# Kernel tuning notes

Hardware: AMD Instinct MI355X
Metric: run time of the kernel (lower is better)

The kernel has to match this reference:

```python
import jax, jax.numpy as jnp
import numpy as np

B, T0, H0, W0 = 16, 8, 14, 14
DIM = 768
HEADS = 8
HD = DIM // HEADS  # 96
N = T0 * H0 * W0 + 1  # 1569 (cls token)
STRIDE_Q = (1, 1, 1)
STRIDE_KV = (1, 2, 2)
REL_SP_DIM = 2 * max(H0, H0 // 2) - 1  # 27
REL_T_DIM = 2 * T0 - 1  # 15
LN_EPS = 1e-5


def _rel_idx(q, k):
    # decomposed relative-position index table (static, numpy)
    q_ratio = max(k / q, 1.0)
    k_ratio = max(q / k, 1.0)
    d = np.arange(q)[:, None] * q_ratio - np.arange(k)[None, :] * k_ratio
    d += (k - 1) * k_ratio
    return d.astype(np.int64)


def _layernorm(x, g, b):
    m = jnp.mean(x, axis=-1, keepdims=True)
    v = jnp.mean((x - m) ** 2, axis=-1, keepdims=True)
    return (x - m) * jax.lax.rsqrt(v + LN_EPS) * g + b


def _attention_pool(t, w, thw, stride, g, b):
    # t: [B, heads, 1+L, C]; depthwise 3x3x3 conv over THW, cls token bypasses pool
    cls_tok, body = t[:, :, :1], t[:, :, 1:]
    Bb, NH, L, C = body.shape
    T, H, W = thw
    x = body.reshape(Bb * NH, T, H, W, C).transpose(0, 4, 1, 2, 3)  # NCDHW
    y = jax.lax.conv_general_dilated(
        x, w, window_strides=stride, padding=[(1, 1), (1, 1), (1, 1)],
        feature_group_count=C, dimension_numbers=('NCDHW', 'OIDHW', 'NCDHW'))
    nT, nH, nW = y.shape[2], y.shape[3], y.shape[4]
    y = y.reshape(Bb, NH, C, nT * nH * nW).transpose(0, 1, 3, 2)
    y = jnp.concatenate([cls_tok, y], axis=2)
    return _layernorm(y, g, b), (nT, nH, nW)


def setup_inputs() -> dict:
    key = jax.random.key(0)
    ks = jax.random.split(key, 12)
    s = 0.02
    inp = {
        'x': jax.random.normal(ks[0], (B, N, DIM), jnp.float32),
        'qkv_w': jax.random.normal(ks[1], (DIM, 3 * DIM), jnp.float32) * s,
        'qkv_b': jax.random.normal(ks[2], (3 * DIM,), jnp.float32) * s,
        'pool_q_w': jax.random.normal(ks[3], (HD, 1, 3, 3, 3), jnp.float32) * s,
        'pool_k_w': jax.random.normal(ks[4], (HD, 1, 3, 3, 3), jnp.float32) * s,
        'pool_v_w': jax.random.normal(ks[5], (HD, 1, 3, 3, 3), jnp.float32) * s,
        'ln_q_g': jnp.ones((HD,), jnp.float32), 'ln_q_b': jnp.zeros((HD,), jnp.float32),
        'ln_k_g': jnp.ones((HD,), jnp.float32), 'ln_k_b': jnp.zeros((HD,), jnp.float32),
        'ln_v_g': jnp.ones((HD,), jnp.float32), 'ln_v_b': jnp.zeros((HD,), jnp.float32),
        'rel_pos_h': jax.random.normal(ks[6], (REL_SP_DIM, HD), jnp.float32) * s,
        'rel_pos_w': jax.random.normal(ks[7], (REL_SP_DIM, HD), jnp.float32) * s,
        'rel_pos_t': jax.random.normal(ks[8], (REL_T_DIM, HD), jnp.float32) * s,
        'proj_w': jax.random.normal(ks[9], (DIM, DIM), jnp.float32) * s,
        'proj_b': jax.random.normal(ks[10], (DIM,), jnp.float32) * s,
        'thw_t': T0, 'thw_h': H0, 'thw_w': W0,
    }
    return inp


def reference(x, qkv_w, qkv_b, pool_q_w, pool_k_w, pool_v_w,
              ln_q_g, ln_q_b, ln_k_g, ln_k_b, ln_v_g, ln_v_b,
              rel_pos_h, rel_pos_w, rel_pos_t, proj_w, proj_b,
              thw_t, thw_h, thw_w):
    thw = (int(thw_t), int(thw_h), int(thw_w))
    Bb, Nn, _ = x.shape
    qkv = (x @ qkv_w + qkv_b).reshape(Bb, Nn, 3, HEADS, HD).transpose(2, 0, 3, 1, 4)
    q, k, v = qkv[0], qkv[1], qkv[2]  # [B, H, N, hd]
    q, q_shape = _attention_pool(q, pool_q_w, thw, STRIDE_Q, ln_q_g, ln_q_b)
    k, k_shape = _attention_pool(k, pool_k_w, thw, STRIDE_KV, ln_k_g, ln_k_b)
    v, _ = _attention_pool(v, pool_v_w, thw, STRIDE_KV, ln_v_g, ln_v_b)
    qt, qh, qw = q_shape
    kt, kh, kw = k_shape
    scale = HD ** -0.5
    attn = jnp.einsum('bhqc,bhkc->bhqk', q * scale, k)  # [B,H,1+Lq,1+Lk]
    # spatial + temporal decomposed relative position bias (cls row/col excluded)
    Rh = rel_pos_h[_rel_idx(qh, kh)]  # [qh,kh,hd]
    Rw = rel_pos_w[_rel_idx(qw, kw)]  # [qw,kw,hd]
    Rt = rel_pos_t[_rel_idx(qt, kt)]  # [qt,kt,hd]
    r_q = q[:, :, 1:].reshape(Bb, HEADS, qt, qh, qw, HD)
    rel_h = jnp.einsum('bythwc,hkc->bythwk', r_q, Rh)  # [B,H,qt,qh,qw,kh]
    rel_w = jnp.einsum('bythwc,wkc->bythwk', r_q, Rw)  # [B,H,qt,qh,qw,kw]
    rel_t = jnp.einsum('bnthwc,tkc->bnthwk', r_q, Rt)  # [B,H,qt,qh,qw,kt]
    bias = (rel_h[:, :, :, :, :, None, :, None]
            + rel_w[:, :, :, :, :, None, None, :]
            + rel_t[:, :, :, :, :, :, None, None])  # [B,H,qt,qh,qw,kt,kh,kw]
    attn = attn.at[:, :, 1:, 1:].add(bias.reshape(Bb, HEADS, qt * qh * qw, kt * kh * kw))
    attn = jax.nn.softmax(attn, axis=-1)
    out = jnp.einsum('bhqk,bhkc->bhqc', attn, v)
    out = out.at[:, :, 1:].add(q[:, :, 1:])  # residual pooling (skip cls)
    out = out.transpose(0, 2, 1, 3).reshape(Bb, -1, DIM)
    out = out @ proj_w + proj_b
    return out
```

## Files before the change

### kernel.cpp

```cpp
#include <hip/hip_runtime.h>
#include <hip/hip_bf16.h>

typedef __hip_bfloat16 bf16;
typedef __attribute__((ext_vector_type(8))) short bf16x8;
typedef __attribute__((ext_vector_type(4))) float f32x4;

#define B_     16
#define N_     1569
#define DIM_   768
#define NHEADS 8
#define HD_    96
#define LK_    393
#define T0_    8
#define H0_    14
#define W0_    14

struct __align__(8) bf16x4s { bf16 a, b, c, d; };

__device__ __forceinline__ float b2f(unsigned short u) {
  union { unsigned int i; float f; } x;
  x.i = ((unsigned int)u) << 16;
  return x.f;
}

__global__ __launch_bounds__(256) void cvt_f32_bf16(
    const float* __restrict__ in, bf16* __restrict__ out, int n4) {
  int i = blockIdx.x * 256 + threadIdx.x;
  if (i < n4) {
    float4 v = ((const float4*)in)[i];
    bf16x4s o{__float2bfloat16(v.x), __float2bfloat16(v.y),
              __float2bfloat16(v.z), __float2bfloat16(v.w)};
    ((bf16x4s*)out)[i] = o;
  }
}

__global__ __launch_bounds__(256) void transpose_f32_bf16(
    const float* __restrict__ in, bf16* __restrict__ out, int R, int C) {
  __shared__ float tile[32][33];
  int c0 = blockIdx.x * 32, r0 = blockIdx.y * 32;
  int tx = threadIdx.x, ty = threadIdx.y;
  for (int i = 0; i < 32; i += 8) {
    int r = r0 + ty + i, c = c0 + tx;
    if (r < R && c < C) tile[ty + i][tx] = in[(size_t)r * C + c];
  }
  __syncthreads();
  for (int i = 0; i < 32; i += 8) {
    int c = c0 + ty + i, r = r0 + tx;
    if (c < C && r < R) out[(size_t)c * R + r] = __float2bfloat16(tile[tx][ty + i]);
  }
}

__global__ __launch_bounds__(256) void prep_pw(
    const float* __restrict__ wq, const float* __restrict__ wk,
    const float* __restrict__ wv, float* __restrict__ outp) {
  int i = blockIdx.x * 256 + threadIdx.x;
  if (i < 2592) {
    int widx = i / 96, x = i % 96;
    outp[i]        = wq[x * 27 + widx];
    outp[2592 + i] = wk[x * 27 + widx];
    outp[5184 + i] = wv[x * 27 + widx];
  }
}

__device__ __forceinline__ void gl_lds16(const bf16* g, bf16* l) {
  __builtin_amdgcn_global_load_lds(
      (const __attribute__((address_space(1))) void*)g,
      (__attribute__((address_space(3))) void*)l, 16, 0, 0);
}

template <typename OutT>
__global__ __launch_bounds__(256) void gemm_bt(
    const bf16* __restrict__ A, const bf16* __restrict__ BT,
    const float* __restrict__ bias, OutT* __restrict__ C,
    int M, int Nn, int K) {
  constexpr int BM = 128, BN = 128, BK = 64;
  __shared__ __align__(16) bf16 As[BM][BK];
  __shared__ __align__(16) bf16 Bs[BN][BK];
  const int tid = threadIdx.x;
  const int lane = tid & 63, wave = tid >> 6;

  const int nNp = Nn >> 7;
  const int nwg = gridDim.x;
  const int q8 = nwg >> 3, r8 = nwg & 7;
  const int xcd = blockIdx.x & 7, idx = blockIdx.x >> 3;
  const int w = (xcd < r8 ? xcd * (q8 + 1) : r8 * (q8 + 1) + (xcd - r8) * q8) + idx;
  const int bm = (w / nNp) * BM, bn = (w % nNp) * BN;

  const int wm = (wave >> 1) * 64, wn = (wave & 1) * 64;
  const int sl = lane >> 3;
  const int sc = ((lane & 7) ^ sl) * 8;

  f32x4 acc[4][4];
#pragma unroll
  for (int i = 0; i < 4; ++i)
#pragma unroll
    for (int j = 0; j < 4; ++j) acc[i][j] = (f32x4){0.f, 0.f, 0.f, 0.f};

  for (int k0 = 0; k0 < K; k0 += BK) {
#pragma unroll
    for (int c = 0; c < 4; ++c) {
      int r0 = wave * 32 + c * 8;
      int arow = bm + r0 + sl;
      if (arow >= M) arow = M - 1;
      gl_lds16(A + (size_t)arow * K + k0 + sc, &As[r0][0]);
      int brow = bn + r0 + sl;
      gl_lds16(BT + (size_t)brow * K + k0 + sc, &Bs[r0][0]);
    }
    __syncthreads();
    const int fr = lane & 15, q = lane >> 4;
#pragma unroll
    for (int ks = 0; ks < 2; ++ks) {
      const int ph = (((ks << 2) + q) ^ (fr & 7)) << 3;
      bf16x8 af[4], bfr[4];
#pragma unroll
      for (int i = 0; i < 4; ++i) {
        af[i] = *(const bf16x8*)&As[wm + i * 16 + fr][ph];
        bfr[i] = *(const bf16x8*)&Bs[wn + i * 16 + fr][ph];
      }
#pragma unroll
      for (int i = 0; i < 4; ++i)
#pragma unroll
        for (int j = 0; j < 4; ++j)
          acc[i][j] = __builtin_amdgcn_mfma_f32_16x16x32_bf16(af[i], bfr[j],
                                                              acc[i][j], 0, 0, 0);
    }
    __syncthreads();
  }

  const int fr = lane & 15, rg = (lane >> 4) * 4;
#pragma unroll
  for (int j = 0; j < 4; ++j) {
    int col = bn + wn + j * 16 + fr;
    float bv = bias[col];
#pragma unroll
    for (int i = 0; i < 4; ++i) {
#pragma unroll
      for (int r = 0; r < 4; ++r) {
        int row = bm + wm + i * 16 + rg + r;
        if (row < M)
          C[(size_t)row * Nn + col] = (OutT)(acc[i][j][r] + bv);
      }
    }
  }
}

__global__ __launch_bounds__(256) void pool_ln(
    const bf16* __restrict__ qkv, const float* __restrict__ pwT,
    const float* __restrict__ g, const float* __restrict__ bt,
    bf16* __restrict__ outp, int which, int sHW, int oH, int oW, int Lout) {
  __shared__ float pwl[27 * 104];
  const int tid = threadIdx.x;
  for (int i = tid; i < 2592; i += 256) {
    int widx = i / 96, c = i % 96;
    int cgi = c >> 3, j = c & 7;
    pwl[widx * 104 + cgi * 8 + (cgi >> 2) * 4 + j] = pwT[i];
  }
  __syncthreads();

  const int rloc = tid >> 4;
  const int cg = tid & 15;
  const int orow = blockIdx.x * 16 + rloc;
  if (orow >= Lout) return;
  const int bh = blockIdx.y;
  const int b = bh >> 3, h = bh & 7;
  const bool act = (cg < 12);
  const bf16* base =
      qkv + (size_t)b * N_ * 2304 + which * 768 + h * 96 + cg * 8;

  float acc[8];
#pragma unroll
  for (int j = 0; j < 8; ++j) acc[j] = 0.f;

  if (act) {
    if (orow == 0) {
      union { uint4 u; bf16 e[8]; } tv;
      tv.u = *(const uint4*)base;
#pragma unroll
      for (int j = 0; j < 8; ++j) acc[j] = (float)tv.e[j];
    } else {
      int pos = orow - 1;
      int ot = pos / (oH * oW), r = pos % (oH * oW);
      int oh = r / oW, ow = r % oW;
      const float* wrow = pwl + cg * 8 + (cg >> 2) * 4;
#pragma unroll
      for (int kt = 0; kt < 3; ++kt) {
        int it = ot + kt - 1;
        if (it < 0 || it >= T0_) continue;
#pragma unroll
        for (int kh = 0; kh < 3; ++kh) {
          int ih = oh * sHW + kh - 1;
          if (ih < 0 || ih >= H0_) continue;
#pragma unroll
          for (int kw = 0; kw < 3; ++kw) {
            int iw = ow * sHW + kw - 1;
            if (iw < 0 || iw >= W0_) continue;
            int n = 1 + (it * H0_ + ih) * W0_ + iw;
            int widx = (kt * 3 + kh) * 3 + kw;
            union { uint4 u; bf16 e[8]; } tv;
            tv.u = *(const uint4*)(base + (size_t)n * 2304);
            const float* w = wrow + widx * 104;
            float wv_[8];
            *(float4*)&wv_[0] = *(const float4*)w;
            *(float4*)&wv_[4] = *(const float4*)(w + 4);
#pragma unroll
            for (int j = 0; j < 8; ++j) acc[j] += (float)tv.e[j] * wv_[j];
          }
        }
      }
    }
  }

  float s = 0.f, s2 = 0.f;
#pragma unroll
  for (int j = 0; j < 8; ++j) { s += acc[j]; s2 += acc[j] * acc[j]; }
#pragma unroll
  for (int mk = 1; mk < 16; mk <<= 1) {
    s += __shfl_xor(s, mk);
    s2 += __shfl_xor(s2, mk);
  }
  float mean = s * (1.f / 96.f);
  float var = s2 * (1.f / 96.f) - mean * mean;
  float rstd = rsqrtf(var + 1e-5f);

  if (act) {
    float gv[8], bv[8];
    *(float4*)&gv[0] = *(const float4*)(g + cg * 8);
    *(float4*)&gv[4] = *(const float4*)(g + cg * 8 + 4);
    *(float4*)&bv[0] = *(const float4*)(bt + cg * 8);
    *(float4*)&bv[4] = *(const float4*)(bt + cg * 8 + 4);
    union { uint4 u; bf16 e[8]; } ov;
#pragma unroll
    for (int j = 0; j < 8; ++j)
      ov.e[j] = __float2bfloat16((acc[j] - mean) * rstd * gv[j] + bv[j]);
    *(uint4*)(outp + ((size_t)bh * Lout + orow) * 96 + cg * 8) = ov.u;
  }
}

__global__ __launch_bounds__(256) void vtran(
    const bf16* __restrict__ vp, bf16* __restrict__ vt) {
  __shared__ __align__(16) bf16 tile[64][104];
  const int tid = threadIdx.x;
  const int bh = blockIdx.y, kt0 = blockIdx.x * 64;
  const bf16* src = vp + (size_t)bh * LK_ * HD_;
  for (int c = tid; c < 768; c += 256) {
    int row = c / 12, seg = c % 12;
    int key = kt0 + row;
    uint4 v = {0u, 0u, 0u, 0u};
    if (key < LK_) v = *(const uint4*)(src + (size_t)key * HD_ + seg * 8);
    *(uint4*)&tile[row][seg * 8] = v;
  }
  __syncthreads();
  bf16* dst = vt + (size_t)bh * 96 * 448 + kt0;
  for (int c = tid; c < 768; c += 256) {
    int d = c >> 3, ch = c & 7;
    union { uint4 u; bf16 e[8]; } o;
#pragma unroll
    for (int j = 0; j < 8; ++j) o.e[j] = tile[ch * 8 + j][d];
    *(uint4*)(dst + (size_t)d * 448 + ch * 8) = o.u;
  }
}

__global__ __launch_bounds__(256) void rel_dots(
    const bf16* __restrict__ qp, const float* __restrict__ rpt,
    const float* __restrict__ rph, const float* __restrict__ rpw,
    float* __restrict__ relq) {
  __shared__ float tab[69 * 100];
  __shared__ __align__(16) bf16 Qls[64][96];
  const int tid = threadIdx.x;
  const int bh = blockIdx.y;
  const int q0 = blockIdx.x * 64;
  const bf16* qb = qp + (size_t)bh * N_ * HD_;

  for (int i = tid; i < 69 * 24; i += 256) {
    int row = i / 24, c4 = (i % 24) * 4;
    const float* src = row < 15 ? rpt + row * 96
                      : row < 42 ? rph + (row - 15) * 96
                                 : rpw + (row - 42) * 96;
    *(float4*)&tab[row * 100 + c4] = *(const float4*)(src + c4);
  }
  for (int c = tid; c < 768; c += 256) {
    int row = c / 12, seg = c % 12;
    int p = q0 + row;
    if (p >= N_) p = N_ - 1;
    *(uint4*)&Qls[row][seg * 8] = *(const uint4*)(qb + (size_t)p * HD_ + seg * 8);
  }
  __syncthreads();

  const int r8 = tid >> 5, slot = tid & 31;
  if (slot == 15 || slot >= 23) return;
  for (int g = 0; g < 8; ++g) {
    int row = g * 8 + r8;
    int p = q0 + row;
    if (p < 1 || p >= N_) continue;
    int pos = p - 1;
    int qt = pos / 196, rr = pos % 196;
    int qh = rr / 14, qw = rr % 14;
    int ti = slot < 8 ? qt - slot + 7
            : slot < 15 ? 15 + (qh - 2 * (slot - 8) + 12)
                        : 42 + (qw - 2 * (slot - 16) + 12);
    const float* trow = &tab[ti * 100];
    float acc = 0.f;
#pragma unroll
    for (int d4 = 0; d4 < 24; ++d4) {
      float4 w = *(const float4*)(trow + d4 * 4);
      union { uint2 u; unsigned short s[4]; } qv;
      qv.u = *(const uint2*)&Qls[row][d4 * 4];
      acc += w.x * b2f(qv.s[0]) + w.y * b2f(qv.s[1]) +
             w.z * b2f(qv.s[2]) + w.w * b2f(qv.s[3]);
    }
    relq[((size_t)bh * N_ + p) * 24 + slot] = acc;
  }
}

__global__ __launch_bounds__(256) void attn_fused(
    const bf16* __restrict__ qp, const bf16* __restrict__ kp,
    const bf16* __restrict__ vtb, const float* __restrict__ relq,
    bf16* __restrict__ aout) {
  __shared__ __align__(16) char smem[31744];
  bf16 (*Ks)[104]    = (bf16(*)[104])smem;
  bf16* VtS          = (bf16*)(smem + 13312);
  float (*relb)[24]  = (float(*)[24])(smem + 25600);
  bf16 (*Ps)[16][72] = (bf16(*)[16][72])smem;

  const int tid = threadIdx.x;
  const int wv = tid >> 6, lane = tid & 63;
  const int col = lane & 15, quad = lane >> 4;
  const int bh = blockIdx.y;
  const int b = bh >> 3;
  const int h = bh & 7;
  const int q0 = blockIdx.x * 64;
  const bf16* qb = qp + (size_t)bh * N_ * HD_;
  const bf16* kb = kp + (size_t)bh * LK_ * HD_;
  const bf16* vt = vtb + (size_t)bh * 96 * 448;
  const float scale = 0.102062072615966f;

  {
    int nrow = N_ - q0;
    if (nrow > 64) nrow = 64;
    int n4 = nrow * 6;
    const uint4* src = (const uint4*)(relq + ((size_t)bh * N_ + q0) * 24);
    for (int i = tid; i < n4; i += 256) ((uint4*)relb)[i] = src[i];
  }

  int qrow = q0 + wv * 16 + col;
  if (qrow >= N_) qrow = N_ - 1;
  bf16x8 qa[3];
#pragma unroll
  for (int ks_ = 0; ks_ < 3; ++ks_)
    qa[ks_] = *(const bf16x8*)(qb + (size_t)qrow * HD_ + ks_ * 32 + quad * 8);

  float mrun[4] = {-1e30f, -1e30f, -1e30f, -1e30f};
  float lrun[4] = {0.f, 0.f, 0.f, 0.f};
  f32x4 oacc[6];
#pragma unroll
  for (int dt = 0; dt < 6; ++dt) oacc[dt] = (f32x4){0.f, 0.f, 0.f, 0.f};

  for (int kt_i = 0; kt_i < 7; ++kt_i) {
    const int kt0 = kt_i * 64;
    __syncthreads();
    for (int c = tid; c < 768; c += 256) {
      int row = c / 12, seg = c % 12;
      int key = kt0 + row;
      if (key >= LK_) key = LK_ - 1;
      *(uint4*)&Ks[row][seg * 8] =
          *(const uint4*)(kb + (size_t)key * HD_ + seg * 8);
    }
    for (int c = tid; c < 768; c += 256) {
      int d = c >> 3, ch = c & 7;
      int c_ = (d ^ (d >> 3)) & 7;
      *(uint4*)&VtS[d * 64 + ch * 8] =
          *(const uint4*)(vt + (size_t)d * 448 + kt0 + ((ch ^ c_) * 8));
    }
    __syncthreads();

    f32x4 sacc[4];
#pragma unroll
    for (int jt = 0; jt < 4; ++jt) sacc[jt] = (f32x4){0.f, 0.f, 0.f, 0.f};
#pragma unroll
    for (int ks_ = 0; ks_ < 3; ++ks_) {
#pragma unroll
      for (int jt = 0; jt < 4; ++jt) {
        bf16x8 bk = *(const bf16x8*)&Ks[jt * 16 + col][ks_ * 32 + quad * 8];
        sacc[jt] = __builtin_amdgcn_mfma_f32_16x16x32_bf16(qa[ks_], bk, sacc[jt], 0, 0, 0);
      }
    }

    float sv[4][4];
#pragma unroll
    for (int jt = 0; jt < 4; ++jt) {
      int kglob = kt0 + jt * 16 + col;
      bool kvalid = (kglob < LK_);
      int kbod = (kglob >= 1) ? kglob - 1 : 0;
      int kt_ = kbod / 49, krem = kbod % 49;
      int kh_ = krem / 7, kw_ = krem % 7;
#pragma unroll
      for (int r = 0; r < 4; ++r) {
        int qr = wv * 16 + quad * 4 + r;
        int p = q0 + qr;
        float s = sacc[jt][r] * scale;
        if (kvalid && kglob >= 1 && p >= 1 && p < N_)
          s += relb[qr][kt_] + relb[qr][8 + kh_] + relb[qr][16 + kw_];
        if (!kvalid) s = -1e30f;
        sv[jt][r] = s;
      }
    }

    float pexp[4][4];
#pragma unroll
    for (int r = 0; r < 4; ++r) {
      float pm = fmaxf(fmaxf(sv[0][r], sv[1][r]), fmaxf(sv[2][r], sv[3][r]));
#pragma unroll
      for (int mk = 1; mk < 16; mk <<= 1) pm = fmaxf(pm, __shfl_xor(pm, mk));
      float mn = fmaxf(mrun[r], pm);
      float alpha = __expf(mrun[r] - mn);
      mrun[r] = mn;
      float rs = 0.f;
#pragma unroll
      for (int jt = 0; jt < 4; ++jt) {
        float e = __expf(sv[jt][r] - mn);
        pexp[jt][r] = e;
        rs += e;
      }
#pragma unroll
      for (int mk = 1; mk < 16; mk <<= 1) rs += __shfl_xor(rs, mk);
      lrun[r] = lrun[r] * alpha + rs;
#pragma unroll
      for (int dt = 0; dt < 6; ++dt) {
        oacc[dt][r] *= alpha;
      }
    }

    __syncthreads();

#pragma unroll
    for (int jt = 0; jt < 4; ++jt)
#pragma unroll
      for (int r = 0; r < 4; ++r)
        Ps[wv][quad * 4 + r][jt * 16 + col] = __float2bfloat16(pexp[jt][r]);

#pragma unroll
    for (int ks_ = 0; ks_ < 2; ++ks_) {
      bf16x8 ap = *(const bf16x8*)&Ps[wv][col][ks_ * 32 + quad * 8];
#pragma unroll
      for (int dt = 0; dt < 6; ++dt) {
        int d = dt * 16 + col;
        int c_ = (d ^ (d >> 3)) & 7;
        bf16x8 bv =
            *(const bf16x8*)&VtS[d * 64 + ((ks_ * 32 + quad * 8) ^ (c_ << 3))];
        oacc[dt] = __builtin_amdgcn_mfma_f32_16x16x32_bf16(ap, bv, oacc[dt], 0, 0, 0);
      }
    }
  }

#pragma unroll
  for (int r = 0; r < 4; ++r) {
    int qr = wv * 16 + quad * 4 + r;
    int p = q0 + qr;
    if (p >= N_) continue;
    float inv = 1.f / lrun[r];
#pragma unroll
    for (int dt = 0; dt < 6; ++dt) {
      int d = dt * 16 + col;
      float val = oacc[dt][r] * inv;
      if (p >= 1) val += (float)qb[(size_t)p * HD_ + d];
      aout[((size_t)b * N_ + p) * DIM_ + h * HD_ + d] = __float2bfloat16(val);
    }
  }
}

extern "C" void kernel_launch(void* const* d_in, const int* in_sizes, int n_in,
                              void* d_out, int out_size, void* d_ws,
                              size_t ws_size, hipStream_t stream) {
  (void)in_sizes; (void)n_in; (void)out_size; (void)ws_size;
  const float* x      = (const float*)d_in[0];
  const float* qkv_w  = (const float*)d_in[1];
  const float* qkv_b  = (const float*)d_in[2];
  const float* pool_q = (const float*)d_in[3];
  const float* pool_k = (const float*)d_in[4];
  const float* pool_v = (const float*)d_in[5];
  const float* ln_q_g = (const float*)d_in[6];
  const float* ln_q_b = (const float*)d_in[7];
  const float* ln_k_g = (const float*)d_in[8];
  const float* ln_k_b = (const float*)d_in[9];
  const float* ln_v_g = (const float*)d_in[10];
  const float* ln_v_b = (const float*)d_in[11];
  const float* rph    = (const float*)d_in[12];
  const float* rpw    = (const float*)d_in[13];
  const float* rpt    = (const float*)d_in[14];
  const float* proj_w = (const float*)d_in[15];
  const float* proj_b = (const float*)d_in[16];

  char* ws = (char*)d_ws;
  bf16* wt_qkv  = (bf16*)(ws);
  bf16* wt_proj = (bf16*)(ws + 3538944);
  bf16* xb      = (bf16*)(ws + 4718592);
  bf16* aout    = xb;
  bf16* qkv     = (bf16*)(ws + 43278336);
  float* relq   = (float*)(ws + 43278336);
  bf16* vtb     = (bf16*)(ws + 63278336);
  bf16* qpoolb  = (bf16*)(ws + 158957568);
  bf16* kpoolb  = (bf16*)(ws + 197517312);
  bf16* vpoolb  = (bf16*)(ws + 207175680);
  float* pwT    = (float*)(ws + 216834048);
  float* outp   = (float*)d_out;

  int n4 = (B_ * N_ * DIM_) / 4;
  cvt_f32_bf16<<<(n4 + 255) / 256, 256, 0, stream>>>(x, xb, n4);
  transpose_f32_bf16<<<dim3(72, 24), dim3(32, 8), 0, stream>>>(qkv_w, wt_qkv, 768, 2304);
  transpose_f32_bf16<<<dim3(24, 24), dim3(32, 8), 0, stream>>>(proj_w, wt_proj, 768, 768);
  prep_pw<<<11, 256, 0, stream>>>(pool_q, pool_k, pool_v, pwT);

  gemm_bt<bf16><<<197 * 18, 256, 0, stream>>>(xb, wt_qkv, qkv_b, qkv,
                                              B_ * N_, 3 * DIM_, DIM_);

  pool_ln<<<dim3(99, 128), 256, 0, stream>>>(qkv, pwT, ln_q_g, ln_q_b, qpoolb,
                                             0, 1, 14, 14, N_);
  pool_ln<<<dim3(25, 128), 256, 0, stream>>>(qkv, pwT + 2592, ln_k_g, ln_k_b,
                                             kpoolb, 1, 2, 7, 7, LK_);
  pool_ln<<<dim3(25, 128), 256, 0, stream>>>(qkv, pwT + 5184, ln_v_g, ln_v_b,
                                             vpoolb, 2, 2, 7, 7, LK_);

  vtran<<<dim3(7, 128), 256, 0, stream>>>(vpoolb, vtb);
  rel_dots<<<dim3(25, 128), 256, 0, stream>>>(qpoolb, rpt, rph, rpw, relq);

  attn_fused<<<dim3(25, 128), 256, 0, stream>>>(qpoolb, kpoolb, vtb, relq,
                                                aout);

  gemm_bt<float><<<197 * 6, 256, 0, stream>>>(aout, wt_proj, proj_b, outp,
                                              B_ * N_, DIM_, DIM_);
}
```

Baseline: 827.2 us.

## Load K and V^T MFMA operands directly from global, drop LDS staging and block barriers

The attention kernel no longer stages K and transposed V tiles in shared memory. Each wave loads its MFMA B-operands straight from global memory, relying on L1/L2 since the per-head K/V is small. All __syncthreads are removed: relb is now loaded per wave for its own rows, and Ps is per wave. This cuts LDS traffic, barrier stalls and LDS footprint, which may raise occupancy. The cost is that the four waves each fetch the same K/V data redundantly through cache, and the loads are less coalesced.

```diff
diff --git a/kernel.cpp b/kernel.cpp
--- a/kernel.cpp
+++ b/kernel.cpp
@@ -316,11 +316,8 @@
     const bf16* __restrict__ qp, const bf16* __restrict__ kp,
     const bf16* __restrict__ vtb, const float* __restrict__ relq,
     bf16* __restrict__ aout) {
-  __shared__ __align__(16) char smem[31744];
-  bf16 (*Ks)[104]    = (bf16(*)[104])smem;
-  bf16* VtS          = (bf16*)(smem + 13312);
-  float (*relb)[24]  = (float(*)[24])(smem + 25600);
-  bf16 (*Ps)[16][72] = (bf16(*)[16][72])smem;
+  __shared__ __align__(16) bf16 Ps[4][16][72];
+  __shared__ __align__(16) float relb[64][28];
 
   const int tid = threadIdx.x;
   const int wv = tid >> 6, lane = tid & 63;
@@ -335,11 +332,15 @@
   const float scale = 0.102062072615966f;
 
   {
-    int nrow = N_ - q0;
-    if (nrow > 64) nrow = 64;
-    int n4 = nrow * 6;
-    const uint4* src = (const uint4*)(relq + ((size_t)bh * N_ + q0) * 24);
-    for (int i = tid; i < n4; i += 256) ((uint4*)relb)[i] = src[i];
+    const int rbase = wv * 16;
+    for (int i = lane; i < 96; i += 64) {
+      int rr = i / 6, c4 = i % 6;
+      int p = q0 + rbase + rr;
+      if (p < N_) {
+        uint4 v = *(const uint4*)(relq + ((size_t)bh * N_ + p) * 24 + c4 * 4);
+        *(uint4*)&relb[rbase + rr][c4 * 4] = v;
+      }
+    }
   }
 
   int qrow = q0 + wv * 16 + col;
@@ -357,32 +358,39 @@
 
   for (int kt_i = 0; kt_i < 7; ++kt_i) {
     const int kt0 = kt_i * 64;
-    __syncthreads();
-    for (int c = tid; c < 768; c += 256) {
-      int row = c / 12, seg = c % 12;
-      int key = kt0 + row;
-      if (key >= LK_) key = LK_ - 1;
-      *(uint4*)&Ks[row][seg * 8] =
-          *(const uint4*)(kb + (size_t)key * HD_ + seg * 8);
-    }
-    for (int c = tid; c < 768; c += 256) {
-      int d = c >> 3, ch = c & 7;
-      int c_ = (d ^ (d >> 3)) & 7;
-      *(uint4*)&VtS[d * 64 + ch * 8] =
-          *(const uint4*)(vt + (size_t)d * 448 + kt0 + ((ch ^ c_) * 8));
-    }
-    __syncthreads();
-
+
+    const bf16* kr0;
+    const bf16* kr1;
+    const bf16* kr2;
+    const bf16* kr3;
+    {
+      int k0g = kt0 + col;
+      int k1g = k0g + 16, k2g = k0g + 32, k3g = k0g + 48;
+      if (k3g > LK_ - 1) {
+        if (k0g > LK_ - 1) k0g = LK_ - 1;
+        if (k1g > LK_ - 1) k1g = LK_ - 1;
+        if (k2g > LK_ - 1) k2g = LK_ - 1;
+        k3g = LK_ - 1;
+      }
+      kr0 = kb + (size_t)k0g * HD_;
+      kr1 = kb + (size_t)k1g * HD_;
+      kr2 = kb + (size_t)k2g * HD_;
+      kr3 = kb + (size_t)k3g * HD_;
+    }
     f32x4 sacc[4];
 #pragma unroll
     for (int jt = 0; jt < 4; ++jt) sacc[jt] = (f32x4){0.f, 0.f, 0.f, 0.f};
 #pragma unroll
     for (int ks_ = 0; ks_ < 3; ++ks_) {
-#pragma unroll
-      for (int jt = 0; jt < 4; ++jt) {
-        bf16x8 bk = *(const bf16x8*)&Ks[jt * 16 + col][ks_ * 32 + quad * 8];
-        sacc[jt] = __builtin_amdgcn_mfma_f32_16x16x32_bf16(qa[ks_], bk, sacc[jt], 0, 0, 0);
-      }
+      const int ko = ks_ * 32 + quad * 8;
+      bf16x8 b0 = *(const bf16x8*)(kr0 + ko);
+      bf16x8 b1 = *(const bf16x8*)(kr1 + ko);
+      bf16x8 b2 = *(const bf16x8*)(kr2 + ko);
+      bf16x8 b3 = *(const bf16x8*)(kr3 + ko);
+      sacc[0] = __builtin_amdgcn_mfma_f32_16x16x32_bf16(qa[ks_], b0, sacc[0], 0, 0, 0);
+      sacc[1] = __builtin_amdgcn_mfma_f32_16x16x32_bf16(qa[ks_], b1, sacc[1], 0, 0, 0);
+      sacc[2] = __builtin_amdgcn_mfma_f32_16x16x32_bf16(qa[ks_], b2, sacc[2], 0, 0, 0);
+      sacc[3] = __builtin_amdgcn_mfma_f32_16x16x32_bf16(qa[ks_], b3, sacc[3], 0, 0, 0);
     }
 
     float sv[4][4];
@@ -430,8 +438,6 @@
       }
     }
 
-    __syncthreads();
-
 #pragma unroll
     for (int jt = 0; jt < 4; ++jt)
 #pragma unroll
@@ -441,12 +447,10 @@
 #pragma unroll
     for (int ks_ = 0; ks_ < 2; ++ks_) {
       bf16x8 ap = *(const bf16x8*)&Ps[wv][col][ks_ * 32 + quad * 8];
+      const int vo = kt0 + ks_ * 32 + quad * 8;
 #pragma unroll
       for (int dt = 0; dt < 6; ++dt) {
-        int d = dt * 16 + col;
-        int c_ = (d ^ (d >> 3)) & 7;
-        bf16x8 bv =
-            *(const bf16x8*)&VtS[d * 64 + ((ks_ * 32 + quad * 8) ^ (c_ << 3))];
+        bf16x8 bv = *(const bf16x8*)(vt + (size_t)(dt * 16 + col) * 448 + vo);
         oacc[dt] = __builtin_amdgcn_mfma_f32_16x16x32_bf16(ap, bv, oacc[dt], 0, 0, 0);
       }
     }
```

After: 831.2 us. No clear change (+0.5%).
